# Kernel optimization log

Hardware: AMD Instinct MI355X
Metric: run time of the kernel (lower is better)

The kernel has to match this reference:

```python
import jax, jax.numpy as jnp
import numpy as np

N_ATOMS = 100000
N_BONDS = 200000
MAX_NB = 6
N_ATOM_FEATS = 39
N_BOND_FEATS = 11
HIDDEN = 128
DEPTH = 6


def setup_inputs() -> dict:
    key = jax.random.key(0)
    k = jax.random.split(key, 8)
    fatoms = jax.random.normal(k[0], (N_ATOMS, N_ATOM_FEATS), dtype=jnp.float32)
    fbonds = jax.random.normal(k[1], (N_BONDS, N_ATOM_FEATS + N_BOND_FEATS), dtype=jnp.float32)
    agraph = jax.random.randint(k[2], (N_ATOMS, MAX_NB), 0, N_BONDS, dtype=jnp.int32)
    bgraph = jax.random.randint(k[3], (N_BONDS, MAX_NB), 0, N_BONDS, dtype=jnp.int32)
    s_i = 1.0 / np.sqrt(N_ATOM_FEATS + N_BOND_FEATS)
    s_h = 1.0 / np.sqrt(HIDDEN)
    s_o = 1.0 / np.sqrt(N_ATOM_FEATS + HIDDEN)
    W_i = jax.random.uniform(k[4], (HIDDEN, N_ATOM_FEATS + N_BOND_FEATS), jnp.float32, -s_i, s_i)
    W_h = jax.random.uniform(k[5], (HIDDEN, HIDDEN), jnp.float32, -s_h, s_h)
    W_o = jax.random.uniform(k[6], (HIDDEN, N_ATOM_FEATS + HIDDEN), jnp.float32, -s_o, s_o)
    b_o = jax.random.uniform(k[7], (HIDDEN,), jnp.float32, -s_o, s_o)
    return {"fatoms": fatoms, "fbonds": fbonds, "agraph": agraph, "bgraph": bgraph,
            "W_i": W_i, "W_h": W_h, "W_o": W_o, "b_o": b_o}


def reference(fatoms, fbonds, agraph, bgraph, W_i, W_h, W_o, b_o):
    # Input message per directed bond: [n_bonds, hidden]
    binput = fbonds @ W_i.T
    message = jax.nn.relu(binput)
    # Message passing: gather neighbor bond messages, sum, linear, residual-add input, ReLU
    for _ in range(DEPTH - 1):
        nei = jnp.take(message, bgraph, axis=0).sum(axis=1)   # [n_bonds, hidden]
        message = jax.nn.relu(binput + nei @ W_h.T)
    # Aggregate incoming bond messages per atom
    a_nei = jnp.take(message, agraph, axis=0).sum(axis=1)      # [n_atoms, hidden]
    atom_input = jnp.concatenate([fatoms, a_nei], axis=1)      # dropout is identity at eval
    atom_h = jax.nn.relu(atom_input @ W_o.T + b_o)
    return atom_h
```

## Files before the change

kernel.cpp:

```cpp
#include <hip/hip_runtime.h>

#define N_ATOMS   100000
#define N_BONDS   200000
#define MAX_NB    6
#define AF        39
#define BFEAT     50
#define H         128
#define DEPTH     6
#define KS_I      2
#define KS_IH     6
#define KS_O      6
#define FBW       64
#define FAW       64

typedef unsigned short ushort_t;
typedef unsigned int   uint_t;

typedef __attribute__((ext_vector_type(8))) short  bf16x8;
typedef __attribute__((ext_vector_type(4))) float  f32x4;

__device__ inline uint_t cvt_pk(float lo, float hi) {
    uint_t r;
    asm("v_cvt_pk_bf16_f32 %0, %1, %2" : "=v"(r) : "v"(lo), "v"(hi));
    return r;
}
__device__ inline ushort_t f2bf(float f) { return (ushort_t)cvt_pk(f, f); }

__device__ inline void addv(float* a, uint4 v) {
    union { uint_t u; float f; } c;
    c.u = v.x << 16;          a[0] += c.f;
    c.u = v.x & 0xffff0000u;  a[1] += c.f;
    c.u = v.y << 16;          a[2] += c.f;
    c.u = v.y & 0xffff0000u;  a[3] += c.f;
    c.u = v.z << 16;          a[4] += c.f;
    c.u = v.z & 0xffff0000u;  a[5] += c.f;
    c.u = v.w << 16;          a[6] += c.f;
    c.u = v.w & 0xffff0000u;  a[7] += c.f;
}

__global__ __launch_bounds__(256) void k_pack(const float* __restrict__ W_i,
                                              const float* __restrict__ W_h,
                                              const float* __restrict__ W_o,
                                              ushort_t* __restrict__ pWi,
                                              ushort_t* __restrict__ pWih,
                                              ushort_t* __restrict__ pWo) {
    int id = blockIdx.x * 256 + threadIdx.x;
    int mat;
    ushort_t* dst;
    if (id < 1024)      { mat = 0; dst = pWi; }
    else if (id < 4096) { mat = 1; dst = pWih; id -= 1024; }
    else                { mat = 2; dst = pWo;  id -= 4096; }
    const int lane = id & 63;
    const int nt   = (id >> 6) & 7;
    const int ks   = id >> 9;
    const int n  = nt * 16 + (lane & 15);
    const int k0 = ks * 32 + (lane >> 4) * 8;
    float v[8];
#pragma unroll
    for (int j = 0; j < 8; ++j) {
        const int k = k0 + j;
        float x = 0.f;
        if (mat == 0) {
            if (k < BFEAT) x = W_i[n * BFEAT + k];
        } else if (mat == 1) {
            if (k < BFEAT)     x = W_i[n * BFEAT + k];
            else if (k >= FBW) x = W_h[n * H + (k - FBW)];
        } else {
            if (k < H)           x = W_o[(size_t)n * (AF + H) + AF + k];
            else if (k < H + AF) x = W_o[(size_t)n * (AF + H) + (k - H)];
        }
        v[j] = x;
    }
    uint4 u;
    u.x = cvt_pk(v[0], v[1]); u.y = cvt_pk(v[2], v[3]);
    u.z = cvt_pk(v[4], v[5]); u.w = cvt_pk(v[6], v[7]);
    ((uint4*)dst)[id] = u;
}

__global__ __launch_bounds__(256) void k_fab(const float* __restrict__ fatoms,
                                             ushort_t* __restrict__ fab) {
    const int t = threadIdx.x;
    const int a0 = blockIdx.x * 64;
    const int row = t >> 2;
    const int c0 = (t & 3) * 16;
    const int a = a0 + row;
    if (a >= N_ATOMS) return;
    float v[16];
#pragma unroll
    for (int j = 0; j < 16; ++j) {
        const int c = c0 + j;
        v[j] = (c < AF) ? fatoms[(size_t)a * AF + c] : 0.f;
    }
    uint4 u0, u1;
    u0.x = cvt_pk(v[0],  v[1]);  u0.y = cvt_pk(v[2],  v[3]);
    u0.z = cvt_pk(v[4],  v[5]);  u0.w = cvt_pk(v[6],  v[7]);
    u1.x = cvt_pk(v[8],  v[9]);  u1.y = cvt_pk(v[10], v[11]);
    u1.z = cvt_pk(v[12], v[13]); u1.w = cvt_pk(v[14], v[15]);
    *(uint4*)(fab + (size_t)a * FAW + c0)     = u0;
    *(uint4*)(fab + (size_t)a * FAW + c0 + 8) = u1;
}

__global__ __launch_bounds__(256) void k_binput(const float* __restrict__ fbonds,
                                                const ushort_t* __restrict__ pWi,
                                                ushort_t* __restrict__ fbb,
                                                ushort_t* __restrict__ msg0) {
    __shared__ __align__(16) ushort_t sAC[64][136];
    const int t = threadIdx.x;
    const int b0 = blockIdx.x * 64;

    for (int i = t; i < 64 * 25; i += 256) {
        const int row = i / 25, j = i % 25;
        const float2 v = *(const float2*)(fbonds + (size_t)(b0 + row) * BFEAT + j * 2);
        *(uint_t*)&sAC[row][j * 2] = cvt_pk(v.x, v.y);
    }
    for (int i = t; i < 64 * 7; i += 256) {
        const int row = i / 7, c = BFEAT + (i % 7) * 2;
        *(uint_t*)&sAC[row][c] = 0u;
    }
    __syncthreads();

    for (int i = t; i < 64 * 8; i += 256) {
        const int row = i >> 3, c0 = (i & 7) * 8;
        *(uint4*)(fbb + (size_t)(b0 + row) * FBW + c0) = *(const uint4*)&sAC[row][c0];
    }

    const int w    = t >> 6;
    const int lane = t & 63;
    const int col  = lane & 15;
    const int kg   = lane >> 4;
    const int m    = 16 * w + col;

    f32x4 acc[8];
#pragma unroll
    for (int nt = 0; nt < 8; ++nt) acc[nt] = (f32x4){0.f, 0.f, 0.f, 0.f};
    bf16x8 af[KS_I];
#pragma unroll
    for (int ks = 0; ks < KS_I; ++ks)
        af[ks] = *(const bf16x8*)&sAC[m][ks * 32 + kg * 8];
#pragma unroll
    for (int ks = 0; ks < KS_I; ++ks) {
#pragma unroll
        for (int nt = 0; nt < 8; ++nt) {
            const bf16x8 b = *(const bf16x8*)(pWi + (((size_t)(ks * 8 + nt) * 64 + lane) * 8));
            acc[nt] = __builtin_amdgcn_mfma_f32_16x16x32_bf16(af[ks], b, acc[nt], 0, 0, 0);
        }
    }
    __syncthreads();

    const int row0 = kg * 4;
#pragma unroll
    for (int nt = 0; nt < 8; ++nt)
#pragma unroll
        for (int r = 0; r < 4; ++r)
            sAC[16 * w + row0 + r][nt * 16 + col] = f2bf(fmaxf(acc[nt][r], 0.f));
    __syncthreads();

    for (int i = t; i < 64 * 16; i += 256) {
        const int row = i >> 4, c0 = (i & 15) * 8;
        *(uint4*)(msg0 + (size_t)(b0 + row) * H + c0) = *(const uint4*)&sAC[row][c0];
    }
}

__global__ __launch_bounds__(256) void k_mp(const ushort_t* __restrict__ msg_in,
                                            const int* __restrict__ bgraph,
                                            const ushort_t* __restrict__ pWih,
                                            const ushort_t* __restrict__ fbb,
                                            ushort_t* __restrict__ msg_out) {
    __shared__ __align__(16) ushort_t sAC[64][136];
    __shared__ int sIdx[64][MAX_NB];
    const int t = threadIdx.x;
    const int b0 = blockIdx.x * 64;

    for (int i = t; i < 64 * MAX_NB; i += 256)
        sIdx[i / MAX_NB][i % MAX_NB] = bgraph[(size_t)b0 * MAX_NB + i];
    __syncthreads();

    {
        const int bi = t >> 4;
        const int c0 = (t & 15) * 8;
#pragma unroll
        for (int p = 0; p < 4; p += 2) {
            const int iA = p * 16 + bi;
            const int iB = iA + 16;
            uint4 vA[MAX_NB], vB[MAX_NB];
#pragma unroll
            for (int j = 0; j < MAX_NB; ++j)
                vA[j] = *(const uint4*)(msg_in + (size_t)sIdx[iA][j] * H + c0);
#pragma unroll
            for (int j = 0; j < MAX_NB; ++j)
                vB[j] = *(const uint4*)(msg_in + (size_t)sIdx[iB][j] * H + c0);
            float a[8], b[8];
#pragma unroll
            for (int q = 0; q < 8; ++q) { a[q] = 0.f; b[q] = 0.f; }
#pragma unroll
            for (int j = 0; j < MAX_NB; ++j) addv(a, vA[j]);
#pragma unroll
            for (int j = 0; j < MAX_NB; ++j) addv(b, vB[j]);
            uint4 ua, ub;
            ua.x = cvt_pk(a[0], a[1]); ua.y = cvt_pk(a[2], a[3]);
            ua.z = cvt_pk(a[4], a[5]); ua.w = cvt_pk(a[6], a[7]);
            ub.x = cvt_pk(b[0], b[1]); ub.y = cvt_pk(b[2], b[3]);
            ub.z = cvt_pk(b[4], b[5]); ub.w = cvt_pk(b[6], b[7]);
            *(uint4*)&sAC[iA][c0] = ua;
            *(uint4*)&sAC[iB][c0] = ub;
        }
    }

    const int w    = t >> 6;
    const int lane = t & 63;
    const int col  = lane & 15;
    const int kg   = lane >> 4;
    const int m    = 16 * w + col;

    bf16x8 af[KS_IH];
    af[0] = *(const bf16x8*)(fbb + (size_t)(b0 + m) * FBW + kg * 8);
    af[1] = *(const bf16x8*)(fbb + (size_t)(b0 + m) * FBW + 32 + kg * 8);
    __syncthreads();
#pragma unroll
    for (int ks = 2; ks < KS_IH; ++ks)
        af[ks] = *(const bf16x8*)&sAC[m][(ks - 2) * 32 + kg * 8];

    f32x4 acc[8];
#pragma unroll
    for (int nt = 0; nt < 8; ++nt) acc[nt] = (f32x4){0.f, 0.f, 0.f, 0.f};
#pragma unroll
    for (int ks = 0; ks < KS_IH; ++ks) {
#pragma unroll
        for (int nt = 0; nt < 8; ++nt) {
            const bf16x8 b = *(const bf16x8*)(pWih + (((size_t)(ks * 8 + nt) * 64 + lane) * 8));
            acc[nt] = __builtin_amdgcn_mfma_f32_16x16x32_bf16(af[ks], b, acc[nt], 0, 0, 0);
        }
    }
    const int row0 = kg * 4;
#pragma unroll
    for (int nt = 0; nt < 8; ++nt)
#pragma unroll
        for (int r = 0; r < 4; ++r)
            sAC[16 * w + row0 + r][nt * 16 + col] = f2bf(fmaxf(acc[nt][r], 0.f));
    __syncthreads();

    for (int i = t; i < 64 * 16; i += 256) {
        const int row = i >> 4, c0 = (i & 15) * 8;
        *(uint4*)(msg_out + (size_t)(b0 + row) * H + c0) = *(const uint4*)&sAC[row][c0];
    }
}

__global__ __launch_bounds__(256) void k_out(const ushort_t* __restrict__ msg,
                                             const int* __restrict__ agraph,
                                             const ushort_t* __restrict__ fab,
                                             const ushort_t* __restrict__ pWo,
                                             const float* __restrict__ b_o,
                                             float* __restrict__ out) {
    __shared__ __align__(16) ushort_t sA[64][136];
    __shared__ int sIdx[64][MAX_NB];
    const int t = threadIdx.x;
    const int a0 = blockIdx.x * 64;

    for (int i = t; i < 64 * MAX_NB; i += 256) {
        const int a = a0 + i / MAX_NB;
        sIdx[i / MAX_NB][i % MAX_NB] = (a < N_ATOMS) ? agraph[(size_t)a * MAX_NB + (i % MAX_NB)] : 0;
    }
    __syncthreads();

    {
        const int bi = t >> 4;
        const int c0 = (t & 15) * 8;
#pragma unroll
        for (int p = 0; p < 4; p += 2) {
            const int iA = p * 16 + bi;
            const int iB = iA + 16;
            uint4 vA[MAX_NB], vB[MAX_NB];
#pragma unroll
            for (int j = 0; j < MAX_NB; ++j)
                vA[j] = *(const uint4*)(msg + (size_t)sIdx[iA][j] * H + c0);
#pragma unroll
            for (int j = 0; j < MAX_NB; ++j)
                vB[j] = *(const uint4*)(msg + (size_t)sIdx[iB][j] * H + c0);
            float a[8], b[8];
#pragma unroll
            for (int q = 0; q < 8; ++q) { a[q] = 0.f; b[q] = 0.f; }
#pragma unroll
            for (int j = 0; j < MAX_NB; ++j) addv(a, vA[j]);
#pragma unroll
            for (int j = 0; j < MAX_NB; ++j) addv(b, vB[j]);
            uint4 ua, ub;
            ua.x = cvt_pk(a[0], a[1]); ua.y = cvt_pk(a[2], a[3]);
            ua.z = cvt_pk(a[4], a[5]); ua.w = cvt_pk(a[6], a[7]);
            ub.x = cvt_pk(b[0], b[1]); ub.y = cvt_pk(b[2], b[3]);
            ub.z = cvt_pk(b[4], b[5]); ub.w = cvt_pk(b[6], b[7]);
            *(uint4*)&sA[iA][c0] = ua;
            *(uint4*)&sA[iB][c0] = ub;
        }
    }

    const int w    = t >> 6;
    const int lane = t & 63;
    const int col  = lane & 15;
    const int kg   = lane >> 4;
    const int m    = 16 * w + col;
    const int am   = a0 + m;
    const size_t amc = (size_t)((am < N_ATOMS) ? am : 0);

    bf16x8 af[KS_O];
    af[4] = *(const bf16x8*)(fab + amc * FAW + kg * 8);
    af[5] = *(const bf16x8*)(fab + amc * FAW + 32 + kg * 8);
    __syncthreads();
#pragma unroll
    for (int ks = 0; ks < 4; ++ks)
        af[ks] = *(const bf16x8*)&sA[m][ks * 32 + kg * 8];

    f32x4 acc[8];
#pragma unroll
    for (int nt = 0; nt < 8; ++nt) acc[nt] = (f32x4){0.f, 0.f, 0.f, 0.f};
#pragma unroll
    for (int ks = 0; ks < KS_O; ++ks) {
#pragma unroll
        for (int nt = 0; nt < 8; ++nt) {
            const bf16x8 b = *(const bf16x8*)(pWo + (((size_t)(ks * 8 + nt) * 64 + lane) * 8));
            acc[nt] = __builtin_amdgcn_mfma_f32_16x16x32_bf16(af[ks], b, acc[nt], 0, 0, 0);
        }
    }

    float bias[8];
#pragma unroll
    for (int nt = 0; nt < 8; ++nt) bias[nt] = b_o[nt * 16 + col];
    const int rowbase = a0 + 16 * w + kg * 4;
#pragma unroll
    for (int nt = 0; nt < 8; ++nt) {
#pragma unroll
        for (int r = 0; r < 4; ++r) {
            const int arow = rowbase + r;
            if (arow < N_ATOMS)
                out[(size_t)arow * H + nt * 16 + col] = fmaxf(acc[nt][r] + bias[nt], 0.f);
        }
    }
}

extern "C" void kernel_launch(void* const* d_in, const int* in_sizes, int n_in,
                              void* d_out, int out_size, void* d_ws, size_t ws_size,
                              hipStream_t stream) {
    const float* fatoms = (const float*)d_in[0];
    const float* fbonds = (const float*)d_in[1];
    const int*   agraph = (const int*)d_in[2];
    const int*   bgraph = (const int*)d_in[3];
    const float* W_i    = (const float*)d_in[4];
    const float* W_h    = (const float*)d_in[5];
    const float* W_o    = (const float*)d_in[6];
    const float* b_o    = (const float*)d_in[7];
    float* out = (float*)d_out;

    const size_t MSG_BYTES = (size_t)N_BONDS * H * sizeof(ushort_t);
    const size_t FBB_BYTES = (size_t)N_BONDS * FBW * sizeof(ushort_t);
    const size_t FAB_BYTES = (size_t)N_ATOMS * FAW * sizeof(ushort_t);
    char* ws = (char*)d_ws;
    ushort_t* m0   = (ushort_t*)(ws);
    ushort_t* m1   = (ushort_t*)(ws + MSG_BYTES);
    ushort_t* fbb  = (ushort_t*)(ws + 2 * MSG_BYTES);
    ushort_t* fab  = (ushort_t*)(ws + 2 * MSG_BYTES + FBB_BYTES);
    char*     wb   = ws + 2 * MSG_BYTES + FBB_BYTES + FAB_BYTES;
    ushort_t* pWi  = (ushort_t*)(wb);
    ushort_t* pWih = (ushort_t*)(wb + 16 * 1024);
    ushort_t* pWo  = (ushort_t*)(wb + 64 * 1024);

    k_pack<<<28, 256, 0, stream>>>(W_i, W_h, W_o, pWi, pWih, pWo);
    k_fab<<<(N_ATOMS + 63) / 64, 256, 0, stream>>>(fatoms, fab);
    k_binput<<<N_BONDS / 64, 256, 0, stream>>>(fbonds, pWi, fbb, m0);

    ushort_t* cur = m0;
    ushort_t* nxt = m1;
    for (int d = 0; d < DEPTH - 1; ++d) {
        k_mp<<<N_BONDS / 64, 256, 0, stream>>>(cur, bgraph, pWih, fbb, nxt);
        ushort_t* tmp = cur; cur = nxt; nxt = tmp;
    }

    k_out<<<(N_ATOMS + 63) / 64, 256, 0, stream>>>(cur, agraph, fab, pWo, b_o, out);
}
```

Before: 467.0 us.

## Persistent message-passing kernel with prefetched gathers and precomputed binput accumulator

The message-passing kernel becomes persistent with a grid of 1024 blocks. Each block loads W_h into shared memory once and software-pipelines the neighbor gathers and bgraph index loads for the next tile while computing the current tile. The W_i·fbonds product is now computed once in k_binput and stored as a bf16 accumulator in MFMA-fragment layout, which shrinks the per-step GEMM K from 192 to 128. Outputs are written straight from registers with strided 2-byte stores rather than staged through LDS. The trade-offs are higher register pressure from 24 prefetched uint4 values, extra rounding of binput to bf16, and scattered narrow stores.

```diff
diff --git a/kernel.cpp b/kernel.cpp
--- a/kernel.cpp
+++ b/kernel.cpp
@@ -8,10 +8,11 @@
 #define H         128
 #define DEPTH     6
 #define KS_I      2
-#define KS_IH     6
+#define KS_H      4
 #define KS_O      6
-#define FBW       64
 #define FAW       64
+#define NTILES    (N_BONDS / 64)
+#define GMP       1024
 
 typedef unsigned short ushort_t;
 typedef unsigned int   uint_t;
@@ -25,31 +26,34 @@
     return r;
 }
 __device__ inline ushort_t f2bf(float f) { return (ushort_t)cvt_pk(f, f); }
+__device__ inline float bflo(uint_t u) { union { uint_t i; float f; } v; v.i = u << 16; return v.f; }
+__device__ inline float bfhi(uint_t u) { union { uint_t i; float f; } v; v.i = u & 0xffff0000u; return v.f; }
 
 __device__ inline void addv(float* a, uint4 v) {
-    union { uint_t u; float f; } c;
-    c.u = v.x << 16;          a[0] += c.f;
-    c.u = v.x & 0xffff0000u;  a[1] += c.f;
-    c.u = v.y << 16;          a[2] += c.f;
-    c.u = v.y & 0xffff0000u;  a[3] += c.f;
-    c.u = v.z << 16;          a[4] += c.f;
-    c.u = v.z & 0xffff0000u;  a[5] += c.f;
-    c.u = v.w << 16;          a[6] += c.f;
-    c.u = v.w & 0xffff0000u;  a[7] += c.f;
+    a[0] += bflo(v.x); a[1] += bfhi(v.x);
+    a[2] += bflo(v.y); a[3] += bfhi(v.y);
+    a[4] += bflo(v.z); a[5] += bfhi(v.z);
+    a[6] += bflo(v.w); a[7] += bfhi(v.w);
+}
+
+__device__ inline void barx() {
+    asm volatile("s_waitcnt lgkmcnt(0)" ::: "memory");
+    __builtin_amdgcn_s_barrier();
+    __builtin_amdgcn_sched_barrier(0);
 }
 
 __global__ __launch_bounds__(256) void k_pack(const float* __restrict__ W_i,
                                               const float* __restrict__ W_h,
                                               const float* __restrict__ W_o,
                                               ushort_t* __restrict__ pWi,
-                                              ushort_t* __restrict__ pWih,
+                                              ushort_t* __restrict__ pWh,
                                               ushort_t* __restrict__ pWo) {
     int id = blockIdx.x * 256 + threadIdx.x;
     int mat;
     ushort_t* dst;
     if (id < 1024)      { mat = 0; dst = pWi; }
-    else if (id < 4096) { mat = 1; dst = pWih; id -= 1024; }
-    else                { mat = 2; dst = pWo;  id -= 4096; }
+    else if (id < 3072) { mat = 1; dst = pWh; id -= 1024; }
+    else                { mat = 2; dst = pWo; id -= 3072; }
     const int lane = id & 63;
     const int nt   = (id >> 6) & 7;
     const int ks   = id >> 9;
@@ -60,12 +64,9 @@
     for (int j = 0; j < 8; ++j) {
         const int k = k0 + j;
         float x = 0.f;
-        if (mat == 0) {
-            if (k < BFEAT) x = W_i[n * BFEAT + k];
-        } else if (mat == 1) {
-            if (k < BFEAT)     x = W_i[n * BFEAT + k];
-            else if (k >= FBW) x = W_h[n * H + (k - FBW)];
-        } else {
+        if (mat == 0)      { if (k < BFEAT) x = W_i[n * BFEAT + k]; }
+        else if (mat == 1) { x = W_h[n * H + k]; }
+        else {
             if (k < H)           x = W_o[(size_t)n * (AF + H) + AF + k];
             else if (k < H + AF) x = W_o[(size_t)n * (AF + H) + (k - H)];
         }
@@ -102,7 +103,7 @@
 
 __global__ __launch_bounds__(256) void k_binput(const float* __restrict__ fbonds,
                                                 const ushort_t* __restrict__ pWi,
-                                                ushort_t* __restrict__ fbb,
+                                                ushort_t* __restrict__ bP,
                                                 ushort_t* __restrict__ msg0) {
     __shared__ __align__(16) ushort_t sAC[64][136];
     const int t = threadIdx.x;
@@ -118,11 +119,6 @@
         *(uint_t*)&sAC[row][c] = 0u;
     }
     __syncthreads();
-
-    for (int i = t; i < 64 * 8; i += 256) {
-        const int row = i >> 3, c0 = (i & 7) * 8;
-        *(uint4*)(fbb + (size_t)(b0 + row) * FBW + c0) = *(const uint4*)&sAC[row][c0];
-    }
 
     const int w    = t >> 6;
     const int lane = t & 63;
@@ -145,7 +141,22 @@
             acc[nt] = __builtin_amdgcn_mfma_f32_16x16x32_bf16(af[ks], b, acc[nt], 0, 0, 0);
         }
     }
-    __syncthreads();
+
+    {
+        uint_t u[16];
+#pragma unroll
+        for (int nt = 0; nt < 8; ++nt) {
+            u[nt * 2]     = cvt_pk(acc[nt][0], acc[nt][1]);
+            u[nt * 2 + 1] = cvt_pk(acc[nt][2], acc[nt][3]);
+        }
+        uint4* base = (uint4*)bP + (size_t)(blockIdx.x * 4 + w) * 256 + lane;
+#pragma unroll
+        for (int i = 0; i < 4; ++i) {
+            uint4 q;
+            q.x = u[4 * i]; q.y = u[4 * i + 1]; q.z = u[4 * i + 2]; q.w = u[4 * i + 3];
+            base[i * 64] = q;
+        }
+    }
 
     const int row0 = kg * 4;
 #pragma unroll
@@ -163,85 +174,115 @@
 
 __global__ __launch_bounds__(256) void k_mp(const ushort_t* __restrict__ msg_in,
                                             const int* __restrict__ bgraph,
-                                            const ushort_t* __restrict__ pWih,
-                                            const ushort_t* __restrict__ fbb,
+                                            const ushort_t* __restrict__ pWh,
+                                            const ushort_t* __restrict__ binputP,
                                             ushort_t* __restrict__ msg_out) {
-    __shared__ __align__(16) ushort_t sAC[64][136];
-    __shared__ int sIdx[64][MAX_NB];
+    __shared__ __align__(16) ushort_t sA[64][136];
+    __shared__ __align__(16) ushort_t sWh[KS_H * 8 * 64 * 8];
+    __shared__ __align__(16) int sIdx[2][64 * MAX_NB];
     const int t = threadIdx.x;
-    const int b0 = blockIdx.x * 64;
-
-    for (int i = t; i < 64 * MAX_NB; i += 256)
-        sIdx[i / MAX_NB][i % MAX_NB] = bgraph[(size_t)b0 * MAX_NB + i];
-    __syncthreads();
+    const int bi = t >> 4;
+    const int c0 = (t & 15) * 8;
+    const int w = t >> 6, lane = t & 63, col = lane & 15, kg = lane >> 4;
+    const int m = 16 * w + col;
+    const int G = GMP;
+
+    int tile = blockIdx.x;
 
     {
-        const int bi = t >> 4;
-        const int c0 = (t & 15) * 8;
-#pragma unroll
-        for (int p = 0; p < 4; p += 2) {
-            const int iA = p * 16 + bi;
-            const int iB = iA + 16;
-            uint4 vA[MAX_NB], vB[MAX_NB];
-#pragma unroll
-            for (int j = 0; j < MAX_NB; ++j)
-                vA[j] = *(const uint4*)(msg_in + (size_t)sIdx[iA][j] * H + c0);
-#pragma unroll
-            for (int j = 0; j < MAX_NB; ++j)
-                vB[j] = *(const uint4*)(msg_in + (size_t)sIdx[iB][j] * H + c0);
-            float a[8], b[8];
-#pragma unroll
-            for (int q = 0; q < 8; ++q) { a[q] = 0.f; b[q] = 0.f; }
-#pragma unroll
-            for (int j = 0; j < MAX_NB; ++j) addv(a, vA[j]);
-#pragma unroll
-            for (int j = 0; j < MAX_NB; ++j) addv(b, vB[j]);
-            uint4 ua, ub;
-            ua.x = cvt_pk(a[0], a[1]); ua.y = cvt_pk(a[2], a[3]);
-            ua.z = cvt_pk(a[4], a[5]); ua.w = cvt_pk(a[6], a[7]);
-            ub.x = cvt_pk(b[0], b[1]); ub.y = cvt_pk(b[2], b[3]);
-            ub.z = cvt_pk(b[4], b[5]); ub.w = cvt_pk(b[6], b[7]);
-            *(uint4*)&sAC[iA][c0] = ua;
-            *(uint4*)&sAC[iB][c0] = ub;
-        }
-    }
-
-    const int w    = t >> 6;
-    const int lane = t & 63;
-    const int col  = lane & 15;
-    const int kg   = lane >> 4;
-    const int m    = 16 * w + col;
-
-    bf16x8 af[KS_IH];
-    af[0] = *(const bf16x8*)(fbb + (size_t)(b0 + m) * FBW + kg * 8);
-    af[1] = *(const bf16x8*)(fbb + (size_t)(b0 + m) * FBW + 32 + kg * 8);
-    __syncthreads();
-#pragma unroll
-    for (int ks = 2; ks < KS_IH; ++ks)
-        af[ks] = *(const bf16x8*)&sAC[m][(ks - 2) * 32 + kg * 8];
-
-    f32x4 acc[8];
-#pragma unroll
-    for (int nt = 0; nt < 8; ++nt) acc[nt] = (f32x4){0.f, 0.f, 0.f, 0.f};
-#pragma unroll
-    for (int ks = 0; ks < KS_IH; ++ks) {
-#pragma unroll
-        for (int nt = 0; nt < 8; ++nt) {
-            const bf16x8 b = *(const bf16x8*)(pWih + (((size_t)(ks * 8 + nt) * 64 + lane) * 8));
-            acc[nt] = __builtin_amdgcn_mfma_f32_16x16x32_bf16(af[ks], b, acc[nt], 0, 0, 0);
-        }
-    }
-    const int row0 = kg * 4;
-#pragma unroll
-    for (int nt = 0; nt < 8; ++nt)
-#pragma unroll
-        for (int r = 0; r < 4; ++r)
-            sAC[16 * w + row0 + r][nt * 16 + col] = f2bf(fmaxf(acc[nt][r], 0.f));
-    __syncthreads();
-
-    for (int i = t; i < 64 * 16; i += 256) {
-        const int row = i >> 4, c0 = (i & 15) * 8;
-        *(uint4*)(msg_out + (size_t)(b0 + row) * H + c0) = *(const uint4*)&sAC[row][c0];
+        const uint4* src = (const uint4*)pWh;
+        uint4* dst = (uint4*)sWh;
+#pragma unroll
+        for (int i = 0; i < 8; ++i) dst[t + i * 256] = src[t + i * 256];
+    }
+    if (t < 96)
+        ((int4*)sIdx[0])[t] = ((const int4*)(bgraph + (size_t)tile * 384))[t];
+    barx();
+
+    uint4 g[24];
+#pragma unroll
+    for (int r = 0; r < 4; ++r)
+#pragma unroll
+        for (int j = 0; j < 6; ++j) {
+            const uint_t off = (uint_t)sIdx[0][(r * 16 + bi) * 6 + j] * H + c0;
+            g[r * 6 + j] = *(const uint4*)(msg_in + off);
+        }
+    int4 idxPF = {0, 0, 0, 0};
+    if (t < 96 && tile + G < NTILES)
+        idxPF = ((const int4*)(bgraph + (size_t)(tile + G) * 384))[t];
+
+    int ib = 1;
+    for (;;) {
+        const int b0 = tile * 64;
+        const uint4* bp4 = (const uint4*)binputP + (size_t)(tile * 4 + w) * 256 + lane;
+        uint4 q0 = bp4[0], q1 = bp4[64], q2 = bp4[128], q3 = bp4[192];
+
+#pragma unroll
+        for (int r = 0; r < 4; ++r) {
+            float a8[8];
+#pragma unroll
+            for (int qq = 0; qq < 8; ++qq) a8[qq] = 0.f;
+#pragma unroll
+            for (int j = 0; j < 6; ++j) addv(a8, g[r * 6 + j]);
+            uint4 u;
+            u.x = cvt_pk(a8[0], a8[1]); u.y = cvt_pk(a8[2], a8[3]);
+            u.z = cvt_pk(a8[4], a8[5]); u.w = cvt_pk(a8[6], a8[7]);
+            *(uint4*)&sA[r * 16 + bi][c0] = u;
+        }
+
+        const bool hasN = (tile + G) < NTILES;
+        if (t < 96 && hasN) ((int4*)sIdx[ib])[t] = idxPF;
+        if (t < 96 && (tile + 2 * G) < NTILES)
+            idxPF = ((const int4*)(bgraph + (size_t)(tile + 2 * G) * 384))[t];
+
+        barx();
+
+        if (hasN) {
+#pragma unroll
+            for (int r = 0; r < 4; ++r)
+#pragma unroll
+                for (int j = 0; j < 6; ++j) {
+                    const uint_t off = (uint_t)sIdx[ib][(r * 16 + bi) * 6 + j] * H + c0;
+                    g[r * 6 + j] = *(const uint4*)(msg_in + off);
+                }
+        }
+
+        bf16x8 af[KS_H];
+#pragma unroll
+        for (int ks = 0; ks < KS_H; ++ks)
+            af[ks] = *(const bf16x8*)&sA[m][ks * 32 + kg * 8];
+
+        barx();
+
+        f32x4 acc[8];
+#pragma unroll
+        for (int i = 0; i < 4; ++i) {
+            const uint4 q = (i == 0) ? q0 : (i == 1) ? q1 : (i == 2) ? q2 : q3;
+            acc[2 * i][0]     = bflo(q.x); acc[2 * i][1]     = bfhi(q.x);
+            acc[2 * i][2]     = bflo(q.y); acc[2 * i][3]     = bfhi(q.y);
+            acc[2 * i + 1][0] = bflo(q.z); acc[2 * i + 1][1] = bfhi(q.z);
+            acc[2 * i + 1][2] = bflo(q.w); acc[2 * i + 1][3] = bfhi(q.w);
+        }
+#pragma unroll
+        for (int ks = 0; ks < KS_H; ++ks)
+#pragma unroll
+            for (int nt = 0; nt < 8; ++nt) {
+                const bf16x8 b = *(const bf16x8*)&sWh[((ks * 8 + nt) * 64 + lane) * 8];
+                acc[nt] = __builtin_amdgcn_mfma_f32_16x16x32_bf16(af[ks], b, acc[nt], 0, 0, 0);
+            }
+
+        const int rowb = b0 + 16 * w + kg * 4;
+#pragma unroll
+        for (int r = 0; r < 4; ++r) {
+            ushort_t* op = msg_out + (size_t)(rowb + r) * H + col;
+#pragma unroll
+            for (int nt = 0; nt < 8; ++nt)
+                op[nt * 16] = f2bf(fmaxf(acc[nt][r], 0.f));
+        }
+
+        tile += G;
+        if (tile >= NTILES) break;
+        ib ^= 1;
     }
 }
 
@@ -350,26 +391,25 @@
     float* out = (float*)d_out;
 
     const size_t MSG_BYTES = (size_t)N_BONDS * H * sizeof(ushort_t);
-    const size_t FBB_BYTES = (size_t)N_BONDS * FBW * sizeof(ushort_t);
     const size_t FAB_BYTES = (size_t)N_ATOMS * FAW * sizeof(ushort_t);
     char* ws = (char*)d_ws;
     ushort_t* m0   = (ushort_t*)(ws);
     ushort_t* m1   = (ushort_t*)(ws + MSG_BYTES);
-    ushort_t* fbb  = (ushort_t*)(ws + 2 * MSG_BYTES);
-    ushort_t* fab  = (ushort_t*)(ws + 2 * MSG_BYTES + FBB_BYTES);
-    char*     wb   = ws + 2 * MSG_BYTES + FBB_BYTES + FAB_BYTES;
+    ushort_t* bP   = (ushort_t*)(ws + 2 * MSG_BYTES);
+    ushort_t* fab  = (ushort_t*)(ws + 3 * MSG_BYTES);
+    char*     wb   = ws + 3 * MSG_BYTES + FAB_BYTES;
     ushort_t* pWi  = (ushort_t*)(wb);
-    ushort_t* pWih = (ushort_t*)(wb + 16 * 1024);
-    ushort_t* pWo  = (ushort_t*)(wb + 64 * 1024);
-
-    k_pack<<<28, 256, 0, stream>>>(W_i, W_h, W_o, pWi, pWih, pWo);
+    ushort_t* pWh  = (ushort_t*)(wb + 16 * 1024);
+    ushort_t* pWo  = (ushort_t*)(wb + 48 * 1024);
+
+    k_pack<<<24, 256, 0, stream>>>(W_i, W_h, W_o, pWi, pWh, pWo);
     k_fab<<<(N_ATOMS + 63) / 64, 256, 0, stream>>>(fatoms, fab);
-    k_binput<<<N_BONDS / 64, 256, 0, stream>>>(fbonds, pWi, fbb, m0);
+    k_binput<<<N_BONDS / 64, 256, 0, stream>>>(fbonds, pWi, bP, m0);
 
     ushort_t* cur = m0;
     ushort_t* nxt = m1;
     for (int d = 0; d < DEPTH - 1; ++d) {
-        k_mp<<<N_BONDS / 64, 256, 0, stream>>>(cur, bgraph, pWih, fbb, nxt);
+        k_mp<<<GMP, 256, 0, stream>>>(cur, bgraph, pWh, bP, nxt);
         ushort_t* tmp = cur; cur = nxt; nxt = tmp;
     }
 
```

Result: slower. 486.4 us (+4.2%).

## Double k_mp bond tile to 128 with 512 threads; stage k_out output via LDS

Applied to the files above, without the earlier changes.

The message-passing kernel now processes 128 bonds per block with 512 threads. Bond indices are loaded as int4 vectors, and the message and feature buffers are padded so the final partial tile stays in bounds. The output kernel stages accumulators through shared memory in two halves, then writes coalesced float4 rows with the bias added. The aim is fewer blocks, vector index loads and coalesced output stores, at the cost of more shared memory per block and extra barriers.

```diff
diff --git a/kernel.cpp b/kernel.cpp
--- a/kernel.cpp
+++ b/kernel.cpp
@@ -2,6 +2,7 @@
 
 #define N_ATOMS   100000
 #define N_BONDS   200000
+#define MSG_ROWS  200064
 #define MAX_NB    6
 #define AF        39
 #define BFEAT     50
@@ -12,6 +13,7 @@
 #define KS_O      6
 #define FBW       64
 #define FAW       64
+#define BMP       128
 
 typedef unsigned short ushort_t;
 typedef unsigned int   uint_t;
@@ -25,17 +27,14 @@
     return r;
 }
 __device__ inline ushort_t f2bf(float f) { return (ushort_t)cvt_pk(f, f); }
+__device__ inline float bflo(uint_t u) { union { uint_t i; float f; } v; v.i = u << 16; return v.f; }
+__device__ inline float bfhi(uint_t u) { union { uint_t i; float f; } v; v.i = u & 0xffff0000u; return v.f; }
 
 __device__ inline void addv(float* a, uint4 v) {
-    union { uint_t u; float f; } c;
-    c.u = v.x << 16;          a[0] += c.f;
-    c.u = v.x & 0xffff0000u;  a[1] += c.f;
-    c.u = v.y << 16;          a[2] += c.f;
-    c.u = v.y & 0xffff0000u;  a[3] += c.f;
-    c.u = v.z << 16;          a[4] += c.f;
-    c.u = v.z & 0xffff0000u;  a[5] += c.f;
-    c.u = v.w << 16;          a[6] += c.f;
-    c.u = v.w & 0xffff0000u;  a[7] += c.f;
+    a[0] += bflo(v.x); a[1] += bfhi(v.x);
+    a[2] += bflo(v.y); a[3] += bfhi(v.y);
+    a[4] += bflo(v.z); a[5] += bfhi(v.z);
+    a[6] += bflo(v.w); a[7] += bfhi(v.w);
 }
 
 __global__ __launch_bounds__(256) void k_pack(const float* __restrict__ W_i,
@@ -161,27 +160,35 @@
     }
 }
 
-__global__ __launch_bounds__(256) void k_mp(const ushort_t* __restrict__ msg_in,
+__global__ __launch_bounds__(512) void k_mp(const ushort_t* __restrict__ msg_in,
                                             const int* __restrict__ bgraph,
                                             const ushort_t* __restrict__ pWih,
                                             const ushort_t* __restrict__ fbb,
                                             ushort_t* __restrict__ msg_out) {
-    __shared__ __align__(16) ushort_t sAC[64][136];
-    __shared__ int sIdx[64][MAX_NB];
+    __shared__ __align__(16) ushort_t sAC[BMP][136];
+    __shared__ __align__(16) int sIdx[BMP][MAX_NB];
     const int t = threadIdx.x;
-    const int b0 = blockIdx.x * 64;
-
-    for (int i = t; i < 64 * MAX_NB; i += 256)
-        sIdx[i / MAX_NB][i % MAX_NB] = bgraph[(size_t)b0 * MAX_NB + i];
+    const int b0 = blockIdx.x * BMP;
+
+    if (b0 + BMP <= N_BONDS) {
+        if (t < 192)
+            ((int4*)sIdx)[t] = ((const int4*)(bgraph + (size_t)b0 * MAX_NB))[t];
+    } else {
+        for (int i = t; i < BMP * MAX_NB; i += 512) {
+            const int row = b0 + i / MAX_NB;
+            sIdx[i / MAX_NB][i % MAX_NB] =
+                (row < N_BONDS) ? bgraph[(size_t)row * MAX_NB + (i % MAX_NB)] : 0;
+        }
+    }
     __syncthreads();
 
     {
-        const int bi = t >> 4;
+        const int rg = t >> 4;
         const int c0 = (t & 15) * 8;
 #pragma unroll
         for (int p = 0; p < 4; p += 2) {
-            const int iA = p * 16 + bi;
-            const int iB = iA + 16;
+            const int iA = p * 32 + rg;
+            const int iB = iA + 32;
             uint4 vA[MAX_NB], vB[MAX_NB];
 #pragma unroll
             for (int j = 0; j < MAX_NB; ++j)
@@ -189,18 +196,18 @@
 #pragma unroll
             for (int j = 0; j < MAX_NB; ++j)
                 vB[j] = *(const uint4*)(msg_in + (size_t)sIdx[iB][j] * H + c0);
-            float a[8], b[8];
-#pragma unroll
-            for (int q = 0; q < 8; ++q) { a[q] = 0.f; b[q] = 0.f; }
-#pragma unroll
-            for (int j = 0; j < MAX_NB; ++j) addv(a, vA[j]);
-#pragma unroll
-            for (int j = 0; j < MAX_NB; ++j) addv(b, vB[j]);
+            float a8[8], b8[8];
+#pragma unroll
+            for (int q = 0; q < 8; ++q) { a8[q] = 0.f; b8[q] = 0.f; }
+#pragma unroll
+            for (int j = 0; j < MAX_NB; ++j) addv(a8, vA[j]);
+#pragma unroll
+            for (int j = 0; j < MAX_NB; ++j) addv(b8, vB[j]);
             uint4 ua, ub;
-            ua.x = cvt_pk(a[0], a[1]); ua.y = cvt_pk(a[2], a[3]);
-            ua.z = cvt_pk(a[4], a[5]); ua.w = cvt_pk(a[6], a[7]);
-            ub.x = cvt_pk(b[0], b[1]); ub.y = cvt_pk(b[2], b[3]);
-            ub.z = cvt_pk(b[4], b[5]); ub.w = cvt_pk(b[6], b[7]);
+            ua.x = cvt_pk(a8[0], a8[1]); ua.y = cvt_pk(a8[2], a8[3]);
+            ua.z = cvt_pk(a8[4], a8[5]); ua.w = cvt_pk(a8[6], a8[7]);
+            ub.x = cvt_pk(b8[0], b8[1]); ub.y = cvt_pk(b8[2], b8[3]);
+            ub.z = cvt_pk(b8[4], b8[5]); ub.w = cvt_pk(b8[6], b8[7]);
             *(uint4*)&sAC[iA][c0] = ua;
             *(uint4*)&sAC[iB][c0] = ub;
         }
@@ -239,7 +246,9 @@
             sAC[16 * w + row0 + r][nt * 16 + col] = f2bf(fmaxf(acc[nt][r], 0.f));
     __syncthreads();
 
-    for (int i = t; i < 64 * 16; i += 256) {
+#pragma unroll
+    for (int p = 0; p < 4; ++p) {
+        const int i = t + p * 512;
         const int row = i >> 4, c0 = (i & 15) * 8;
         *(uint4*)(msg_out + (size_t)(b0 + row) * H + c0) = *(const uint4*)&sAC[row][c0];
     }
@@ -251,7 +260,9 @@
                                              const ushort_t* __restrict__ pWo,
                                              const float* __restrict__ b_o,
                                              float* __restrict__ out) {
-    __shared__ __align__(16) ushort_t sA[64][136];
+    __shared__ __align__(16) unsigned char smem[64 * 136 * 2];
+    ushort_t (*sA)[136] = (ushort_t(*)[136])smem;
+    float    (*sCh)[68] = (float(*)[68])smem;
     __shared__ int sIdx[64][MAX_NB];
     const int t = threadIdx.x;
     const int a0 = blockIdx.x * 64;
@@ -276,18 +287,18 @@
 #pragma unroll
             for (int j = 0; j < MAX_NB; ++j)
                 vB[j] = *(const uint4*)(msg + (size_t)sIdx[iB][j] * H + c0);
-            float a[8], b[8];
-#pragma unroll
-            for (int q = 0; q < 8; ++q) { a[q] = 0.f; b[q] = 0.f; }
-#pragma unroll
-            for (int j = 0; j < MAX_NB; ++j) addv(a, vA[j]);
-#pragma unroll
-            for (int j = 0; j < MAX_NB; ++j) addv(b, vB[j]);
+            float a8[8], b8[8];
+#pragma unroll
+            for (int q = 0; q < 8; ++q) { a8[q] = 0.f; b8[q] = 0.f; }
+#pragma unroll
+            for (int j = 0; j < MAX_NB; ++j) addv(a8, vA[j]);
+#pragma unroll
+            for (int j = 0; j < MAX_NB; ++j) addv(b8, vB[j]);
             uint4 ua, ub;
-            ua.x = cvt_pk(a[0], a[1]); ua.y = cvt_pk(a[2], a[3]);
-            ua.z = cvt_pk(a[4], a[5]); ua.w = cvt_pk(a[6], a[7]);
-            ub.x = cvt_pk(b[0], b[1]); ub.y = cvt_pk(b[2], b[3]);
-            ub.z = cvt_pk(b[4], b[5]); ub.w = cvt_pk(b[6], b[7]);
+            ua.x = cvt_pk(a8[0], a8[1]); ua.y = cvt_pk(a8[2], a8[3]);
+            ua.z = cvt_pk(a8[4], a8[5]); ua.w = cvt_pk(a8[6], a8[7]);
+            ub.x = cvt_pk(b8[0], b8[1]); ub.y = cvt_pk(b8[2], b8[3]);
+            ub.z = cvt_pk(b8[4], b8[5]); ub.w = cvt_pk(b8[6], b8[7]);
             *(uint4*)&sA[iA][c0] = ua;
             *(uint4*)&sA[iB][c0] = ub;
         }
@@ -320,19 +331,32 @@
             acc[nt] = __builtin_amdgcn_mfma_f32_16x16x32_bf16(af[ks], b, acc[nt], 0, 0, 0);
         }
     }
-
-    float bias[8];
-#pragma unroll
-    for (int nt = 0; nt < 8; ++nt) bias[nt] = b_o[nt * 16 + col];
-    const int rowbase = a0 + 16 * w + kg * 4;
-#pragma unroll
-    for (int nt = 0; nt < 8; ++nt) {
-#pragma unroll
-        for (int r = 0; r < 4; ++r) {
-            const int arow = rowbase + r;
-            if (arow < N_ATOMS)
-                out[(size_t)arow * H + nt * 16 + col] = fmaxf(acc[nt][r] + bias[nt], 0.f);
-        }
+    __syncthreads();
+
+    const int row0 = kg * 4;
+    const float4* bo4 = (const float4*)b_o;
+#pragma unroll
+    for (int half = 0; half < 2; ++half) {
+#pragma unroll
+        for (int nt = 0; nt < 4; ++nt)
+#pragma unroll
+            for (int r = 0; r < 4; ++r)
+                sCh[16 * w + row0 + r][nt * 16 + col] = acc[half * 4 + nt][r];
+        __syncthreads();
+#pragma unroll
+        for (int p = 0; p < 4; ++p) {
+            const int i = t + p * 256;
+            const int row = i >> 4, c0 = (i & 15) * 4;
+            const int a = a0 + row;
+            if (a < N_ATOMS) {
+                float4 cv = *(const float4*)&sCh[row][c0];
+                const float4 bv = bo4[(half * 64 + c0) >> 2];
+                cv.x = fmaxf(cv.x + bv.x, 0.f); cv.y = fmaxf(cv.y + bv.y, 0.f);
+                cv.z = fmaxf(cv.z + bv.z, 0.f); cv.w = fmaxf(cv.w + bv.w, 0.f);
+                *(float4*)(out + (size_t)a * H + half * 64 + c0) = cv;
+            }
+        }
+        if (half == 0) __syncthreads();
     }
 }
 
@@ -349,8 +373,8 @@
     const float* b_o    = (const float*)d_in[7];
     float* out = (float*)d_out;
 
-    const size_t MSG_BYTES = (size_t)N_BONDS * H * sizeof(ushort_t);
-    const size_t FBB_BYTES = (size_t)N_BONDS * FBW * sizeof(ushort_t);
+    const size_t MSG_BYTES = (size_t)MSG_ROWS * H * sizeof(ushort_t);
+    const size_t FBB_BYTES = (size_t)MSG_ROWS * FBW * sizeof(ushort_t);
     const size_t FAB_BYTES = (size_t)N_ATOMS * FAW * sizeof(ushort_t);
     char* ws = (char*)d_ws;
     ushort_t* m0   = (ushort_t*)(ws);
@@ -368,8 +392,9 @@
 
     ushort_t* cur = m0;
     ushort_t* nxt = m1;
+    const int gmp = (N_BONDS + BMP - 1) / BMP;
     for (int d = 0; d < DEPTH - 1; ++d) {
-        k_mp<<<N_BONDS / 64, 256, 0, stream>>>(cur, bgraph, pWih, fbb, nxt);
+        k_mp<<<gmp, 512, 0, stream>>>(cur, bgraph, pWih, fbb, nxt);
         ushort_t* tmp = cur; cur = nxt; nxt = tmp;
     }
 
```

Result: slower. 544.2 us (+16.5%).

## Switch intermediates to fp16 with packed-add gathers and LDS-staged output stores

Applied to the files above, without the earlier changes.

Changes every stored intermediate (messages, packed weights, features) from bf16 to fp16 and uses f16 MFMA. Neighbor sums now use packed fp16 adds (v_pk_add_f16) in place of unpacking to fp32 and repacking, which cuts ALU work in the gather-heavy message-passing kernels. The output kernel now stages accumulators through shared memory so it can write coalesced float4 rows instead of scattered scalar stores. The cost is lower dynamic range and fp16 accumulation across six neighbors, which could hurt accuracy or overflow.

```diff
diff --git a/kernel.cpp b/kernel.cpp
--- a/kernel.cpp
+++ b/kernel.cpp
@@ -16,26 +16,25 @@
 typedef unsigned short ushort_t;
 typedef unsigned int   uint_t;
 
-typedef __attribute__((ext_vector_type(8))) short  bf16x8;
-typedef __attribute__((ext_vector_type(4))) float  f32x4;
-
-__device__ inline uint_t cvt_pk(float lo, float hi) {
+typedef __attribute__((ext_vector_type(8))) _Float16 f16x8;
+typedef __attribute__((ext_vector_type(4))) float    f32x4;
+
+__device__ inline uint_t pkh(float lo, float hi) {
     uint_t r;
-    asm("v_cvt_pk_bf16_f32 %0, %1, %2" : "=v"(r) : "v"(lo), "v"(hi));
+    asm("v_cvt_pkrtz_f16_f32 %0, %1, %2" : "=v"(r) : "v"(lo), "v"(hi));
     return r;
 }
-__device__ inline ushort_t f2bf(float f) { return (ushort_t)cvt_pk(f, f); }
-
-__device__ inline void addv(float* a, uint4 v) {
-    union { uint_t u; float f; } c;
-    c.u = v.x << 16;          a[0] += c.f;
-    c.u = v.x & 0xffff0000u;  a[1] += c.f;
-    c.u = v.y << 16;          a[2] += c.f;
-    c.u = v.y & 0xffff0000u;  a[3] += c.f;
-    c.u = v.z << 16;          a[4] += c.f;
-    c.u = v.z & 0xffff0000u;  a[5] += c.f;
-    c.u = v.w << 16;          a[6] += c.f;
-    c.u = v.w & 0xffff0000u;  a[7] += c.f;
+__device__ inline ushort_t f2h(float f) {
+    union { _Float16 h; ushort_t u; } v; v.h = (_Float16)f; return v.u;
+}
+__device__ inline uint_t pkadd(uint_t a, uint_t b) {
+    uint_t r;
+    asm("v_pk_add_f16 %0, %1, %2" : "=v"(r) : "v"(a), "v"(b));
+    return r;
+}
+__device__ inline void addq(uint4& a, uint4 v) {
+    a.x = pkadd(a.x, v.x); a.y = pkadd(a.y, v.y);
+    a.z = pkadd(a.z, v.z); a.w = pkadd(a.w, v.w);
 }
 
 __global__ __launch_bounds__(256) void k_pack(const float* __restrict__ W_i,
@@ -72,8 +71,8 @@
         v[j] = x;
     }
     uint4 u;
-    u.x = cvt_pk(v[0], v[1]); u.y = cvt_pk(v[2], v[3]);
-    u.z = cvt_pk(v[4], v[5]); u.w = cvt_pk(v[6], v[7]);
+    u.x = pkh(v[0], v[1]); u.y = pkh(v[2], v[3]);
+    u.z = pkh(v[4], v[5]); u.w = pkh(v[6], v[7]);
     ((uint4*)dst)[id] = u;
 }
 
@@ -92,10 +91,10 @@
         v[j] = (c < AF) ? fatoms[(size_t)a * AF + c] : 0.f;
     }
     uint4 u0, u1;
-    u0.x = cvt_pk(v[0],  v[1]);  u0.y = cvt_pk(v[2],  v[3]);
-    u0.z = cvt_pk(v[4],  v[5]);  u0.w = cvt_pk(v[6],  v[7]);
-    u1.x = cvt_pk(v[8],  v[9]);  u1.y = cvt_pk(v[10], v[11]);
-    u1.z = cvt_pk(v[12], v[13]); u1.w = cvt_pk(v[14], v[15]);
+    u0.x = pkh(v[0],  v[1]);  u0.y = pkh(v[2],  v[3]);
+    u0.z = pkh(v[4],  v[5]);  u0.w = pkh(v[6],  v[7]);
+    u1.x = pkh(v[8],  v[9]);  u1.y = pkh(v[10], v[11]);
+    u1.z = pkh(v[12], v[13]); u1.w = pkh(v[14], v[15]);
     *(uint4*)(fab + (size_t)a * FAW + c0)     = u0;
     *(uint4*)(fab + (size_t)a * FAW + c0 + 8) = u1;
 }
@@ -111,7 +110,7 @@
     for (int i = t; i < 64 * 25; i += 256) {
         const int row = i / 25, j = i % 25;
         const float2 v = *(const float2*)(fbonds + (size_t)(b0 + row) * BFEAT + j * 2);
-        *(uint_t*)&sAC[row][j * 2] = cvt_pk(v.x, v.y);
+        *(uint_t*)&sAC[row][j * 2] = pkh(v.x, v.y);
     }
     for (int i = t; i < 64 * 7; i += 256) {
         const int row = i / 7, c = BFEAT + (i % 7) * 2;
@@ -133,16 +132,16 @@
     f32x4 acc[8];
 #pragma unroll
     for (int nt = 0; nt < 8; ++nt) acc[nt] = (f32x4){0.f, 0.f, 0.f, 0.f};
-    bf16x8 af[KS_I];
+    f16x8 af[KS_I];
 #pragma unroll
     for (int ks = 0; ks < KS_I; ++ks)
-        af[ks] = *(const bf16x8*)&sAC[m][ks * 32 + kg * 8];
+        af[ks] = *(const f16x8*)&sAC[m][ks * 32 + kg * 8];
 #pragma unroll
     for (int ks = 0; ks < KS_I; ++ks) {
 #pragma unroll
         for (int nt = 0; nt < 8; ++nt) {
-            const bf16x8 b = *(const bf16x8*)(pWi + (((size_t)(ks * 8 + nt) * 64 + lane) * 8));
-            acc[nt] = __builtin_amdgcn_mfma_f32_16x16x32_bf16(af[ks], b, acc[nt], 0, 0, 0);
+            const f16x8 b = *(const f16x8*)(pWi + (((size_t)(ks * 8 + nt) * 64 + lane) * 8));
+            acc[nt] = __builtin_amdgcn_mfma_f32_16x16x32_f16(af[ks], b, acc[nt], 0, 0, 0);
         }
     }
     __syncthreads();
@@ -152,7 +151,7 @@
     for (int nt = 0; nt < 8; ++nt)
 #pragma unroll
         for (int r = 0; r < 4; ++r)
-            sAC[16 * w + row0 + r][nt * 16 + col] = f2bf(fmaxf(acc[nt][r], 0.f));
+            sAC[16 * w + row0 + r][nt * 16 + col] = f2h(fmaxf(acc[nt][r], 0.f));
     __syncthreads();
 
     for (int i = t; i < 64 * 16; i += 256) {
@@ -189,18 +188,11 @@
 #pragma unroll
             for (int j = 0; j < MAX_NB; ++j)
                 vB[j] = *(const uint4*)(msg_in + (size_t)sIdx[iB][j] * H + c0);
-            float a[8], b[8];
-#pragma unroll
-            for (int q = 0; q < 8; ++q) { a[q] = 0.f; b[q] = 0.f; }
-#pragma unroll
-            for (int j = 0; j < MAX_NB; ++j) addv(a, vA[j]);
-#pragma unroll
-            for (int j = 0; j < MAX_NB; ++j) addv(b, vB[j]);
-            uint4 ua, ub;
-            ua.x = cvt_pk(a[0], a[1]); ua.y = cvt_pk(a[2], a[3]);
-            ua.z = cvt_pk(a[4], a[5]); ua.w = cvt_pk(a[6], a[7]);
-            ub.x = cvt_pk(b[0], b[1]); ub.y = cvt_pk(b[2], b[3]);
-            ub.z = cvt_pk(b[4], b[5]); ub.w = cvt_pk(b[6], b[7]);
+            uint4 ua = vA[0], ub = vB[0];
+#pragma unroll
+            for (int j = 1; j < MAX_NB; ++j) addq(ua, vA[j]);
+#pragma unroll
+            for (int j = 1; j < MAX_NB; ++j) addq(ub, vB[j]);
             *(uint4*)&sAC[iA][c0] = ua;
             *(uint4*)&sAC[iB][c0] = ub;
         }
@@ -212,13 +204,13 @@
     const int kg   = lane >> 4;
     const int m    = 16 * w + col;
 
-    bf16x8 af[KS_IH];
-    af[0] = *(const bf16x8*)(fbb + (size_t)(b0 + m) * FBW + kg * 8);
-    af[1] = *(const bf16x8*)(fbb + (size_t)(b0 + m) * FBW + 32 + kg * 8);
+    f16x8 af[KS_IH];
+    af[0] = *(const f16x8*)(fbb + (size_t)(b0 + m) * FBW + kg * 8);
+    af[1] = *(const f16x8*)(fbb + (size_t)(b0 + m) * FBW + 32 + kg * 8);
     __syncthreads();
 #pragma unroll
     for (int ks = 2; ks < KS_IH; ++ks)
-        af[ks] = *(const bf16x8*)&sAC[m][(ks - 2) * 32 + kg * 8];
+        af[ks] = *(const f16x8*)&sAC[m][(ks - 2) * 32 + kg * 8];
 
     f32x4 acc[8];
 #pragma unroll
@@ -227,8 +219,8 @@
     for (int ks = 0; ks < KS_IH; ++ks) {
 #pragma unroll
         for (int nt = 0; nt < 8; ++nt) {
-            const bf16x8 b = *(const bf16x8*)(pWih + (((size_t)(ks * 8 + nt) * 64 + lane) * 8));
-            acc[nt] = __builtin_amdgcn_mfma_f32_16x16x32_bf16(af[ks], b, acc[nt], 0, 0, 0);
+            const f16x8 b = *(const f16x8*)(pWih + (((size_t)(ks * 8 + nt) * 64 + lane) * 8));
+            acc[nt] = __builtin_amdgcn_mfma_f32_16x16x32_f16(af[ks], b, acc[nt], 0, 0, 0);
         }
     }
     const int row0 = kg * 4;
@@ -236,7 +228,7 @@
     for (int nt = 0; nt < 8; ++nt)
 #pragma unroll
         for (int r = 0; r < 4; ++r)
-            sAC[16 * w + row0 + r][nt * 16 + col] = f2bf(fmaxf(acc[nt][r], 0.f));
+            sAC[16 * w + row0 + r][nt * 16 + col] = f2h(fmaxf(acc[nt][r], 0.f));
     __syncthreads();
 
     for (int i = t; i < 64 * 16; i += 256) {
@@ -251,7 +243,9 @@
                                              const ushort_t* __restrict__ pWo,
                                              const float* __restrict__ b_o,
                                              float* __restrict__ out) {
-    __shared__ __align__(16) ushort_t sA[64][136];
+    __shared__ __align__(16) unsigned char smem[64 * 136 * 2];
+    ushort_t (*sA)[136] = (ushort_t(*)[136])smem;
+    float    (*sCh)[68] = (float(*)[68])smem;
     __shared__ int sIdx[64][MAX_NB];
     const int t = threadIdx.x;
     const int a0 = blockIdx.x * 64;
@@ -276,18 +270,11 @@
 #pragma unroll
             for (int j = 0; j < MAX_NB; ++j)
                 vB[j] = *(const uint4*)(msg + (size_t)sIdx[iB][j] * H + c0);
-            float a[8], b[8];
-#pragma unroll
-            for (int q = 0; q < 8; ++q) { a[q] = 0.f; b[q] = 0.f; }
-#pragma unroll
-            for (int j = 0; j < MAX_NB; ++j) addv(a, vA[j]);
-#pragma unroll
-            for (int j = 0; j < MAX_NB; ++j) addv(b, vB[j]);
-            uint4 ua, ub;
-            ua.x = cvt_pk(a[0], a[1]); ua.y = cvt_pk(a[2], a[3]);
-            ua.z = cvt_pk(a[4], a[5]); ua.w = cvt_pk(a[6], a[7]);
-            ub.x = cvt_pk(b[0], b[1]); ub.y = cvt_pk(b[2], b[3]);
-            ub.z = cvt_pk(b[4], b[5]); ub.w = cvt_pk(b[6], b[7]);
+            uint4 ua = vA[0], ub = vB[0];
+#pragma unroll
+            for (int j = 1; j < MAX_NB; ++j) addq(ua, vA[j]);
+#pragma unroll
+            for (int j = 1; j < MAX_NB; ++j) addq(ub, vB[j]);
             *(uint4*)&sA[iA][c0] = ua;
             *(uint4*)&sA[iB][c0] = ub;
         }
@@ -301,13 +288,13 @@
     const int am   = a0 + m;
     const size_t amc = (size_t)((am < N_ATOMS) ? am : 0);
 
-    bf16x8 af[KS_O];
-    af[4] = *(const bf16x8*)(fab + amc * FAW + kg * 8);
-    af[5] = *(const bf16x8*)(fab + amc * FAW + 32 + kg * 8);
+    f16x8 af[KS_O];
+    af[4] = *(const f16x8*)(fab + amc * FAW + kg * 8);
+    af[5] = *(const f16x8*)(fab + amc * FAW + 32 + kg * 8);
     __syncthreads();
 #pragma unroll
     for (int ks = 0; ks < 4; ++ks)
-        af[ks] = *(const bf16x8*)&sA[m][ks * 32 + kg * 8];
+        af[ks] = *(const f16x8*)&sA[m][ks * 32 + kg * 8];
 
     f32x4 acc[8];
 #pragma unroll
@@ -316,23 +303,36 @@
     for (int ks = 0; ks < KS_O; ++ks) {
 #pragma unroll
         for (int nt = 0; nt < 8; ++nt) {
-            const bf16x8 b = *(const bf16x8*)(pWo + (((size_t)(ks * 8 + nt) * 64 + lane) * 8));
-            acc[nt] = __builtin_amdgcn_mfma_f32_16x16x32_bf16(af[ks], b, acc[nt], 0, 0, 0);
-        }
-    }
-
-    float bias[8];
-#pragma unroll
-    for (int nt = 0; nt < 8; ++nt) bias[nt] = b_o[nt * 16 + col];
-    const int rowbase = a0 + 16 * w + kg * 4;
-#pragma unroll
-    for (int nt = 0; nt < 8; ++nt) {
-#pragma unroll
-        for (int r = 0; r < 4; ++r) {
-            const int arow = rowbase + r;
-            if (arow < N_ATOMS)
-                out[(size_t)arow * H + nt * 16 + col] = fmaxf(acc[nt][r] + bias[nt], 0.f);
-        }
+            const f16x8 b = *(const f16x8*)(pWo + (((size_t)(ks * 8 + nt) * 64 + lane) * 8));
+            acc[nt] = __builtin_amdgcn_mfma_f32_16x16x32_f16(af[ks], b, acc[nt], 0, 0, 0);
+        }
+    }
+    __syncthreads();
+
+    const int row0 = kg * 4;
+    const float4* bo4 = (const float4*)b_o;
+#pragma unroll
+    for (int half = 0; half < 2; ++half) {
+#pragma unroll
+        for (int nt = 0; nt < 4; ++nt)
+#pragma unroll
+            for (int r = 0; r < 4; ++r)
+                sCh[16 * w + row0 + r][nt * 16 + col] = acc[half * 4 + nt][r];
+        __syncthreads();
+#pragma unroll
+        for (int p = 0; p < 4; ++p) {
+            const int i = t + p * 256;
+            const int row = i >> 4, c0 = (i & 15) * 4;
+            const int a = a0 + row;
+            if (a < N_ATOMS) {
+                float4 cv = *(const float4*)&sCh[row][c0];
+                const float4 bv = bo4[(half * 64 + c0) >> 2];
+                cv.x = fmaxf(cv.x + bv.x, 0.f); cv.y = fmaxf(cv.y + bv.y, 0.f);
+                cv.z = fmaxf(cv.z + bv.z, 0.f); cv.w = fmaxf(cv.w + bv.w, 0.f);
+                *(float4*)(out + (size_t)a * H + half * 64 + c0) = cv;
+            }
+        }
+        if (half == 0) __syncthreads();
     }
 }
 
```

Measured after the change: 461.8 us, median of 2. No clear change (-1.1%).
